# Performance work log

Measured on AMD Instinct MI355X. Metric: run time of the kernel, lower is better.

## Reference

```python
import jax, jax.numpy as jnp
import numpy as np

B, S, IN, OUT = 4, 2048, 4096, 11008


def setup_inputs() -> dict:
    key = jax.random.key(0)
    k1, k2, k3, k4 = jax.random.split(key, 4)
    x = jax.random.normal(k1, (B, S, IN), dtype=jnp.float32)
    # int8 weight codes (stored as int32 for portability; values in [0,127))
    weight_int8 = jax.random.randint(k2, (OUT, IN), 0, 127, dtype=jnp.int32)
    scale = jax.random.uniform(k3, (OUT,), dtype=jnp.float32) * 0.01 + 1e-4
    bias = jax.random.normal(k4, (OUT,), dtype=jnp.float32)
    return {"x": x, "weight_int8": weight_int8, "scale": scale, "bias": bias}


def reference(x, weight_int8, scale, bias):
    # dequantize: int8 codes -> fp, per-output-row scale (scale.view(-1,1) in torch)
    w = weight_int8.astype(jnp.float32) * scale[:, None]  # [OUT, IN]
    # F.linear(x, w, bias) == x @ w.T + bias
    out = jnp.einsum('bsi,oi->bso', x, w) + bias  # [B, S, OUT]
    return out
```

## Files before the change

### kernel.cpp

```cpp
#include <hip/hip_runtime.h>
#include <hip/hip_bf16.h>
#include <stdint.h>


#define MT 8192
#define KT 4096
#define NT 11008
#define NKT 32
#define MTILES 32
#define NTILES 86
#define CHUNK_A 32768
#define CHUNK_B 16384

typedef __attribute__((ext_vector_type(8))) short short8;
typedef __attribute__((ext_vector_type(4))) float f32x4;
typedef __attribute__((ext_vector_type(4))) int i32x4;
typedef __attribute__((ext_vector_type(16))) int i32x16;
typedef __attribute__((ext_vector_type(16))) char char16;

static __device__ __forceinline__ short f2bf(float f) {
  union { float f; unsigned u; } c; c.f = f;
  unsigned u = c.u;
  return (short)((u + 0x7fffu + ((u >> 16) & 1u)) >> 16);
}

__global__ __launch_bounds__(256) void quant_x_kernel(const float* __restrict__ in,
                                                      char* __restrict__ Aws,
                                                      float* __restrict__ sx) {
  const int m = blockIdx.x;
  const int t = threadIdx.x;
  const float* row = in + (size_t)m * KT + t * 16;
  f32x4 v[4];
  float mx = 0.f;
#pragma unroll
  for (int i = 0; i < 4; i++) {
    v[i] = *(const f32x4*)(row + i * 4);
#pragma unroll
    for (int j = 0; j < 4; j++) mx = fmaxf(mx, fabsf(v[i][j]));
  }
#pragma unroll
  for (int off = 32; off; off >>= 1) mx = fmaxf(mx, __shfl_xor(mx, off));
  __shared__ float smx[4];
  if ((t & 63) == 0) smx[t >> 6] = mx;
  __syncthreads();
  mx = fmaxf(fmaxf(smx[0], smx[1]), fmaxf(smx[2], smx[3]));
  const float inv = 127.0f / mx;
  if (t == 0) sx[m] = mx * (1.0f / 127.0f);
  char16 q;
#pragma unroll
  for (int i = 0; i < 4; i++)
#pragma unroll
    for (int j = 0; j < 4; j++) q[i * 4 + j] = (char)(int)rintf(v[i][j] * inv);
  const int kt = t >> 3, s = (t >> 1) & 3, hi = t & 1;
  const int lane = (m & 31) | (hi << 5);
  const int r32 = (m >> 5) & 7;
  *(char16*)(Aws + ((size_t)(m >> 8) * NKT + kt) * CHUNK_A +
             (r32 * 4 + s) * 1024 + lane * 16) = q;
}

__global__ __launch_bounds__(256) void cvt_w8_kernel(const int* __restrict__ in,
                                                     char* __restrict__ Bws) {
  const int n = blockIdx.x;
  const int t = threadIdx.x;
  const int* s_ = in + (size_t)n * KT + t * 16;
  char16 q;
#pragma unroll
  for (int i = 0; i < 4; i++) {
    i32x4 a = *(const i32x4*)(s_ + i * 4);
#pragma unroll
    for (int j = 0; j < 4; j++) q[i * 4 + j] = (char)a[j];
  }
  const int kt = t >> 3, s = (t >> 1) & 3, hi = t & 1;
  const int lane = (n & 31) | (hi << 5);
  const int c32 = (n >> 5) & 3;
  *(char16*)(Bws + ((size_t)(n >> 7) * NKT + kt) * CHUNK_B +
             (c32 * 4 + s) * 1024 + lane * 16) = q;
}


#define GLD(chunk, j, ldsbase)                                                   \
  __builtin_amdgcn_global_load_lds(                                              \
      (const __attribute__((address_space(1))) void*)((chunk) + (j) * 4096 +     \
                                                      tid * 16),                 \
      (__attribute__((address_space(3))) void*)((ldsbase) + (j) * 4096 +         \
                                                wid * 1024),                     \
      16, 0, 0)

#define GLDA(chunk, dst)                                       \
  do {                                                         \
    GLD(chunk, 0, dst); GLD(chunk, 1, dst);                    \
    GLD(chunk, 2, dst); GLD(chunk, 3, dst);                    \
    GLD(chunk, 4, dst); GLD(chunk, 5, dst);                    \
    GLD(chunk, 6, dst); GLD(chunk, 7, dst);                    \
  } while (0)

#define BAR asm volatile("s_barrier" ::: "memory")
#define VMC0 asm volatile("s_waitcnt vmcnt(0)" ::: "memory")

#define LOADB(B_, src)                                         \
  do {                                                         \
    const char* bb_ = (src) + wc * 8192 + lane * 16;           \
    B_[0][0] = *(const i32x4*)(bb_);                           \
    B_[0][1] = *(const i32x4*)(bb_ + 1024);                    \
    B_[0][2] = *(const i32x4*)(bb_ + 2048);                    \
    B_[0][3] = *(const i32x4*)(bb_ + 3072);                    \
    B_[1][0] = *(const i32x4*)(bb_ + 4096);                    \
    B_[1][1] = *(const i32x4*)(bb_ + 5120);                    \
    B_[1][2] = *(const i32x4*)(bb_ + 6144);                    \
    B_[1][3] = *(const i32x4*)(bb_ + 7168);                    \
  } while (0)

#define LDSL(LAp, s, aset)                                     \
  do {                                                         \
    const char* a_ = (LAp) + albase + (s) * 1024;              \
    aset[0] = *(const i32x4*)(a_);                             \
    aset[1] = *(const i32x4*)(a_ + 4096);                      \
    aset[2] = *(const i32x4*)(a_ + 8192);                      \
    aset[3] = *(const i32x4*)(a_ + 12288);                     \
  } while (0)

#define MMS(aset, BC, s)                                                       \
  do {                                                                         \
    __builtin_amdgcn_s_setprio(1);                                             \
    _Pragma("unroll") for (int mb = 0; mb < 4; mb++)                           \
        _Pragma("unroll") for (int nb = 0; nb < 2; nb++)                       \
            acc[mb][nb] = __builtin_amdgcn_mfma_i32_32x32x32_i8(               \
                aset[mb], BC[nb][s], acc[mb][nb], 0, 0, 0);                    \
    __builtin_amdgcn_s_setprio(0);                                             \
  } while (0)

#define TILE_BODY(BC, BN_)                                                     \
  {                                                                            \
    const char* LA = Lsm + (t & 1) * 32768;                                    \
    if (t + 1 < NKT) LOADB(BN_, Bch + CHUNK_B);                                \
    LDSL(LA, 1, a1);                                                           \
    MMS(a0, BC, 0);                                                            \
    LDSL(LA, 2, a0);                                                           \
    MMS(a1, BC, 1);                                                            \
    LDSL(LA, 3, a1);                                                           \
    MMS(a0, BC, 2);                                                            \
    MMS(a1, BC, 3);                                                            \
    VMC0;                                                                      \
    BAR;                                                                       \
    if (t + 1 < NKT) {                                                         \
      const char* LAn = Lsm + ((t + 1) & 1) * 32768;                           \
      LDSL(LAn, 0, a0);                                                        \
      if (t + 2 < NKT) {                                                       \
        char* dA = Lsm + (t & 1) * 32768;                                      \
        GLDA(Ach + 2 * CHUNK_A, dA);                                           \
      }                                                                        \
    }                                                                          \
    Ach += CHUNK_A;                                                            \
    Bch += CHUNK_B;                                                            \
    ++t;                                                                       \
  }

__global__ __launch_bounds__(256, 2) void gemm_bless(
    const char* __restrict__ Aws, const char* __restrict__ Bws,
    const float* __restrict__ sx, const float* __restrict__ scale,
    const float* __restrict__ bias, float* __restrict__ out) {
  extern __shared__ char Lsm[];
  const int tid = threadIdx.x;
  const int lane = tid & 63;
  const int wid = tid >> 6;
  const int wr = wid >> 1;
  const int wc = wid & 1;

  const int bid = blockIdx.x;
  const int r = bid >> 3;
  const int mt = (bid & 7) * 4 + (r & 3);
  const int nt = r >> 2;

  const char* Ach = Aws + (size_t)mt * NKT * CHUNK_A;
  const char* Bch = Bws + (size_t)nt * NKT * CHUNK_B;

  const int albase = wr * 16384 + lane * 16;

  i32x16 acc[4][2] = {};
  i32x4 a0[4], a1[4], bA[2][4], bB[2][4];

  {
    GLDA(Ach, Lsm);
    LOADB(bA, Bch);
    VMC0;
    BAR;
    GLDA(Ach + CHUNK_A, Lsm + 32768);
    LDSL(Lsm, 0, a0);
  }

  for (int t = 0; t < NKT;) {
    TILE_BODY(bA, bB);
    TILE_BODY(bB, bA);
  }

  const int col_base = nt * 128 + wc * 64 + (lane & 31);
  const int row0 = mt * 256 + wr * 128 + ((lane >> 5) << 2);
#pragma unroll
  for (int mb = 0; mb < 4; mb++) {
    f32x4 sxq[4];
#pragma unroll
    for (int g = 0; g < 4; g++)
      sxq[g] = *(const f32x4*)(sx + row0 + mb * 32 + g * 8);
#pragma unroll
    for (int nb = 0; nb < 2; nb++) {
      const int n = col_base + nb * 32;
      const float sc = scale[n];
      const float bs = bias[n];
#pragma unroll
      for (int g = 0; g < 4; g++)
#pragma unroll
        for (int j = 0; j < 4; j++) {
          const int row = row0 + mb * 32 + g * 8 + j;
          out[(size_t)row * NT + n] =
              (float)acc[mb][nb][g * 4 + j] * (sxq[g][j] * sc) + bs;
        }
    }
  }
}

__global__ __launch_bounds__(256) void gemm_fallback(
    const float* __restrict__ Ap, const int* __restrict__ Bp,
    const float* __restrict__ scale, const float* __restrict__ bias,
    float* __restrict__ out) {
  __shared__ short ldsA[128 * 64];
  __shared__ short ldsB[128 * 64];
  const int tid = threadIdx.x;
  const int lane = tid & 63;
  const int wid = tid >> 6;
  const int nbn = NT / 128;
  const int cpx = ((MT / 128) * nbn) / 8;
  const int bid = blockIdx.x;
  const int wg = (bid & 7) * cpx + (bid >> 3);
  const int brow = (wg / nbn) * 128;
  const int bcol = (wg % nbn) * 128;
  const int wr = wid >> 1, wc = wid & 1;
  f32x4 acc[4][4] = {{{0.f, 0.f, 0.f, 0.f}}};
  const int srow = tid >> 3;
  const int sk8 = (tid & 7) * 8;
  for (int k0 = 0; k0 < KT; k0 += 64) {
    __syncthreads();
#pragma unroll
    for (int p = 0; p < 4; p++) {
      const int row = p * 32 + srow;
      const float* s = Ap + (size_t)(brow + row) * KT + k0 + sk8;
      f32x4 lo = *(const f32x4*)s;
      f32x4 hi = *(const f32x4*)(s + 4);
      short8 v;
#pragma unroll
      for (int j = 0; j < 4; j++) { v[j] = f2bf(lo[j]); v[4 + j] = f2bf(hi[j]); }
      int bo = (row * 64 + sk8) * 2;
      bo ^= ((row & 7) << 4);
      *(short8*)((char*)ldsA + bo) = v;
    }
#pragma unroll
    for (int p = 0; p < 4; p++) {
      const int row = p * 32 + srow;
      const int* s = Bp + (size_t)(bcol + row) * KT + k0 + sk8;
      i32x4 lo = *(const i32x4*)(s);
      i32x4 hi = *(const i32x4*)(s + 4);
      short8 v;
#pragma unroll
      for (int j = 0; j < 4; j++) { v[j] = f2bf((float)lo[j]); v[4 + j] = f2bf((float)hi[j]); }
      int bo = (row * 64 + sk8) * 2;
      bo ^= ((row & 7) << 4);
      *(short8*)((char*)ldsB + bo) = v;
    }
    __syncthreads();
#pragma unroll
    for (int kk = 0; kk < 2; kk++) {
      short8 af[4], bf2[4];
#pragma unroll
      for (int mi = 0; mi < 4; mi++) {
        const int row = wr * 64 + mi * 16 + (lane & 15);
        int bo = (row * 64 + kk * 32 + (lane >> 4) * 8) * 2;
        bo ^= ((row & 7) << 4);
        af[mi] = *(const short8*)((const char*)ldsA + bo);
      }
#pragma unroll
      for (int ni = 0; ni < 4; ni++) {
        const int row = wc * 64 + ni * 16 + (lane & 15);
        int bo = (row * 64 + kk * 32 + (lane >> 4) * 8) * 2;
        bo ^= ((row & 7) << 4);
        bf2[ni] = *(const short8*)((const char*)ldsB + bo);
      }
#pragma unroll
      for (int mi = 0; mi < 4; mi++)
#pragma unroll
        for (int ni = 0; ni < 4; ni++)
          acc[mi][ni] = __builtin_amdgcn_mfma_f32_16x16x32_bf16(af[mi], bf2[ni],
                                                                acc[mi][ni], 0, 0, 0);
    }
  }
#pragma unroll
  for (int ni = 0; ni < 4; ni++) {
    const int n = bcol + wc * 64 + ni * 16 + (lane & 15);
    const float sc = scale[n];
    const float bs = bias[n];
#pragma unroll
    for (int mi = 0; mi < 4; mi++) {
      const int m0 = brow + wr * 64 + mi * 16 + ((lane >> 4) << 2);
#pragma unroll
      for (int j = 0; j < 4; j++)
        out[(size_t)(m0 + j) * NT + n] = acc[mi][ni][j] * sc + bs;
    }
  }
}

extern "C" void kernel_launch(void* const* d_in, const int* in_sizes, int n_in,
                              void* d_out, int out_size, void* d_ws, size_t ws_size,
                              hipStream_t stream) {
  const float* x = (const float*)d_in[0];
  const int* w = (const int*)d_in[1];
  const float* scale = (const float*)d_in[2];
  const float* bias = (const float*)d_in[3];
  float* out = (float*)d_out;

  const size_t a_bytes = (size_t)MTILES * NKT * CHUNK_A;
  const size_t b_bytes = (size_t)NTILES * NKT * CHUNK_B;
  const size_t s_bytes = (size_t)MT * sizeof(float);

  if (ws_size >= a_bytes + b_bytes + s_bytes) {
    char* aw = (char*)d_ws;
    char* bw = aw + a_bytes;
    float* sx = (float*)(bw + b_bytes);
    quant_x_kernel<<<dim3(MT), dim3(256), 0, stream>>>(x, aw, sx);
    cvt_w8_kernel<<<dim3(NT), dim3(256), 0, stream>>>(w, bw);
    hipFuncSetAttribute((const void*)gemm_bless,
                        hipFuncAttributeMaxDynamicSharedMemorySize, 65536);
    gemm_bless<<<dim3(MTILES * NTILES), dim3(256), 65536, stream>>>(
        aw, bw, sx, scale, bias, out);
  } else {
    gemm_fallback<<<dim3((MT / 128) * (NT / 128)), dim3(256), 0, stream>>>(
        x, w, scale, bias, out);
  }
}
```

Before: 521.5 us.

## Replace LDS-staged A tiles with direct global-to-register loads for both operands

Removes the shared-memory staging of A (global_load_lds plus barriers). Each wave now loads its A and B fragments straight from global memory into registers, using a two-slot register double buffer interleaved with the MFMA groups. The aim is to drop the LDS round trip, barrier stalls and the 64KB shared memory allocation. In exchange, A is fetched once per wave rather than once per block, which doubles global/L1 traffic for A. Load latency is also hidden by only about two MFMA groups, and the final iterations prefetch past the end of each tile.

```diff
diff --git a/kernel.cpp b/kernel.cpp
--- a/kernel.cpp
+++ b/kernel.cpp
@@ -78,88 +78,32 @@
 }
 
 
-#define GLD(chunk, j, ldsbase)                                                   \
-  __builtin_amdgcn_global_load_lds(                                              \
-      (const __attribute__((address_space(1))) void*)((chunk) + (j) * 4096 +     \
-                                                      tid * 16),                 \
-      (__attribute__((address_space(3))) void*)((ldsbase) + (j) * 4096 +         \
-                                                wid * 1024),                     \
-      16, 0, 0)
-
-#define GLDA(chunk, dst)                                       \
-  do {                                                         \
-    GLD(chunk, 0, dst); GLD(chunk, 1, dst);                    \
-    GLD(chunk, 2, dst); GLD(chunk, 3, dst);                    \
-    GLD(chunk, 4, dst); GLD(chunk, 5, dst);                    \
-    GLD(chunk, 6, dst); GLD(chunk, 7, dst);                    \
+#define LOADSL(u, A_, B_)                                                \
+  do {                                                                   \
+    const char* ab_ = Abase + (((u) >> 2) * CHUNK_A + ((u)&3) * 1024);   \
+    A_[0] = *(const i32x4*)(ab_);                                        \
+    A_[1] = *(const i32x4*)(ab_ + 4096);                                 \
+    A_[2] = *(const i32x4*)(ab_ + 8192);                                 \
+    A_[3] = *(const i32x4*)(ab_ + 12288);                                \
+    const char* bb_ = Bbase + (((u) >> 2) * CHUNK_B + ((u)&3) * 1024);   \
+    B_[0] = *(const i32x4*)(bb_);                                        \
+    B_[1] = *(const i32x4*)(bb_ + 4096);                                 \
   } while (0)
 
-#define BAR asm volatile("s_barrier" ::: "memory")
-#define VMC0 asm volatile("s_waitcnt vmcnt(0)" ::: "memory")
-
-#define LOADB(B_, src)                                         \
-  do {                                                         \
-    const char* bb_ = (src) + wc * 8192 + lane * 16;           \
-    B_[0][0] = *(const i32x4*)(bb_);                           \
-    B_[0][1] = *(const i32x4*)(bb_ + 1024);                    \
-    B_[0][2] = *(const i32x4*)(bb_ + 2048);                    \
-    B_[0][3] = *(const i32x4*)(bb_ + 3072);                    \
-    B_[1][0] = *(const i32x4*)(bb_ + 4096);                    \
-    B_[1][1] = *(const i32x4*)(bb_ + 5120);                    \
-    B_[1][2] = *(const i32x4*)(bb_ + 6144);                    \
-    B_[1][3] = *(const i32x4*)(bb_ + 7168);                    \
-  } while (0)
-
-#define LDSL(LAp, s, aset)                                     \
-  do {                                                         \
-    const char* a_ = (LAp) + albase + (s) * 1024;              \
-    aset[0] = *(const i32x4*)(a_);                             \
-    aset[1] = *(const i32x4*)(a_ + 4096);                      \
-    aset[2] = *(const i32x4*)(a_ + 8192);                      \
-    aset[3] = *(const i32x4*)(a_ + 12288);                     \
-  } while (0)
-
-#define MMS(aset, BC, s)                                                       \
+#define MMS(A_, B_)                                                            \
   do {                                                                         \
     __builtin_amdgcn_s_setprio(1);                                             \
     _Pragma("unroll") for (int mb = 0; mb < 4; mb++)                           \
         _Pragma("unroll") for (int nb = 0; nb < 2; nb++)                       \
             acc[mb][nb] = __builtin_amdgcn_mfma_i32_32x32x32_i8(               \
-                aset[mb], BC[nb][s], acc[mb][nb], 0, 0, 0);                    \
+                A_[mb], B_[nb], acc[mb][nb], 0, 0, 0);                         \
     __builtin_amdgcn_s_setprio(0);                                             \
   } while (0)
 
-#define TILE_BODY(BC, BN_)                                                     \
-  {                                                                            \
-    const char* LA = Lsm + (t & 1) * 32768;                                    \
-    if (t + 1 < NKT) LOADB(BN_, Bch + CHUNK_B);                                \
-    LDSL(LA, 1, a1);                                                           \
-    MMS(a0, BC, 0);                                                            \
-    LDSL(LA, 2, a0);                                                           \
-    MMS(a1, BC, 1);                                                            \
-    LDSL(LA, 3, a1);                                                           \
-    MMS(a0, BC, 2);                                                            \
-    MMS(a1, BC, 3);                                                            \
-    VMC0;                                                                      \
-    BAR;                                                                       \
-    if (t + 1 < NKT) {                                                         \
-      const char* LAn = Lsm + ((t + 1) & 1) * 32768;                           \
-      LDSL(LAn, 0, a0);                                                        \
-      if (t + 2 < NKT) {                                                       \
-        char* dA = Lsm + (t & 1) * 32768;                                      \
-        GLDA(Ach + 2 * CHUNK_A, dA);                                           \
-      }                                                                        \
-    }                                                                          \
-    Ach += CHUNK_A;                                                            \
-    Bch += CHUNK_B;                                                            \
-    ++t;                                                                       \
-  }
-
-__global__ __launch_bounds__(256, 2) void gemm_bless(
+__global__ __launch_bounds__(256, 2) void gemm_nolds(
     const char* __restrict__ Aws, const char* __restrict__ Bws,
     const float* __restrict__ sx, const float* __restrict__ scale,
     const float* __restrict__ bias, float* __restrict__ out) {
-  extern __shared__ char Lsm[];
   const int tid = threadIdx.x;
   const int lane = tid & 63;
   const int wid = tid >> 6;
@@ -171,26 +115,21 @@
   const int mt = (bid & 7) * 4 + (r & 3);
   const int nt = r >> 2;
 
-  const char* Ach = Aws + (size_t)mt * NKT * CHUNK_A;
-  const char* Bch = Bws + (size_t)nt * NKT * CHUNK_B;
-
-  const int albase = wr * 16384 + lane * 16;
+  const char* Abase = Aws + (size_t)mt * NKT * CHUNK_A + wr * 16384 + lane * 16;
+  const char* Bbase = Bws + (size_t)nt * NKT * CHUNK_B + wc * 8192 + lane * 16;
 
   i32x16 acc[4][2] = {};
-  i32x4 a0[4], a1[4], bA[2][4], bB[2][4];
-
-  {
-    GLDA(Ach, Lsm);
-    LOADB(bA, Bch);
-    VMC0;
-    BAR;
-    GLDA(Ach + CHUNK_A, Lsm + 32768);
-    LDSL(Lsm, 0, a0);
-  }
-
-  for (int t = 0; t < NKT;) {
-    TILE_BODY(bA, bB);
-    TILE_BODY(bB, bA);
+  i32x4 aP[4], bP[2], aQ[4], bQ[2];
+
+  LOADSL(0, aP, bP);
+  LOADSL(1, aQ, bQ);
+
+  for (int t = 0; t < NKT; ++t) {
+    const int u = t * 4;
+    MMS(aP, bP);  LOADSL(u + 2, aP, bP);
+    MMS(aQ, bQ);  LOADSL(u + 3, aQ, bQ);
+    MMS(aP, bP);  LOADSL(u + 4, aP, bP);
+    MMS(aQ, bQ);  LOADSL(u + 5, aQ, bQ);
   }
 
   const int col_base = nt * 128 + wc * 64 + (lane & 31);
@@ -325,9 +264,7 @@
     float* sx = (float*)(bw + b_bytes);
     quant_x_kernel<<<dim3(MT), dim3(256), 0, stream>>>(x, aw, sx);
     cvt_w8_kernel<<<dim3(NT), dim3(256), 0, stream>>>(w, bw);
-    hipFuncSetAttribute((const void*)gemm_bless,
-                        hipFuncAttributeMaxDynamicSharedMemorySize, 65536);
-    gemm_bless<<<dim3(MTILES * NTILES), dim3(256), 65536, stream>>>(
+    gemm_nolds<<<dim3(MTILES * NTILES), dim3(256), 0, stream>>>(
         aw, bw, sx, scale, bias, out);
   } else {
     gemm_fallback<<<dim3((MT / 128) * (NT / 128)), dim3(256), 0, stream>>>(
```

Measured after the change: 540.2 us. 1.04x slower.

## Swap GEMM tile shape to 128x256 and stream B per k-slice

Applied to the files above, without the earlier changes.

The int8 GEMM tile changes from 256 rows by 128 columns to 128 rows by 256 columns. The workspace layouts of quantized x and weights are rearranged to match. Only the smaller A chunk is staged through double-buffered LDS, which halves LDS use. B fragments are now loaded from global memory per k-slice, interleaved with the MFMAs, and a partial vmcnt wait keeps loads in flight across the barrier. The aim is lower LDS pressure and better latency hiding, at the cost of more direct global B traffic per wave and an extra barrier per k-step.

```diff
diff --git a/kernel.cpp b/kernel.cpp
--- a/kernel.cpp
+++ b/kernel.cpp
@@ -7,10 +7,10 @@
 #define KT 4096
 #define NT 11008
 #define NKT 32
-#define MTILES 32
-#define NTILES 86
-#define CHUNK_A 32768
-#define CHUNK_B 16384
+#define ATILES 64
+#define BTILES 43
+#define CHUNK_A 16384
+#define CHUNK_B 32768
 
 typedef __attribute__((ext_vector_type(8))) short short8;
 typedef __attribute__((ext_vector_type(4))) float f32x4;
@@ -53,8 +53,8 @@
     for (int j = 0; j < 4; j++) q[i * 4 + j] = (char)(int)rintf(v[i][j] * inv);
   const int kt = t >> 3, s = (t >> 1) & 3, hi = t & 1;
   const int lane = (m & 31) | (hi << 5);
-  const int r32 = (m >> 5) & 7;
-  *(char16*)(Aws + ((size_t)(m >> 8) * NKT + kt) * CHUNK_A +
+  const int r32 = (m >> 5) & 3;
+  *(char16*)(Aws + ((size_t)(m >> 7) * NKT + kt) * CHUNK_A +
              (r32 * 4 + s) * 1024 + lane * 16) = q;
 }
 
@@ -72,8 +72,8 @@
   }
   const int kt = t >> 3, s = (t >> 1) & 3, hi = t & 1;
   const int lane = (n & 31) | (hi << 5);
-  const int c32 = (n >> 5) & 3;
-  *(char16*)(Bws + ((size_t)(n >> 7) * NKT + kt) * CHUNK_B +
+  const int c32 = (n >> 5) & 7;
+  *(char16*)(Bws + ((size_t)(n >> 8) * NKT + kt) * CHUNK_B +
              (c32 * 4 + s) * 1024 + lane * 16) = q;
 }
 
@@ -90,24 +90,19 @@
   do {                                                         \
     GLD(chunk, 0, dst); GLD(chunk, 1, dst);                    \
     GLD(chunk, 2, dst); GLD(chunk, 3, dst);                    \
-    GLD(chunk, 4, dst); GLD(chunk, 5, dst);                    \
-    GLD(chunk, 6, dst); GLD(chunk, 7, dst);                    \
   } while (0)
 
 #define BAR asm volatile("s_barrier" ::: "memory")
 #define VMC0 asm volatile("s_waitcnt vmcnt(0)" ::: "memory")
-
-#define LOADB(B_, src)                                         \
+#define VMC20 asm volatile("s_waitcnt vmcnt(20)" ::: "memory")
+
+#define LOADB_SL(B_, ct, s)                                    \
   do {                                                         \
-    const char* bb_ = (src) + wc * 8192 + lane * 16;           \
-    B_[0][0] = *(const i32x4*)(bb_);                           \
-    B_[0][1] = *(const i32x4*)(bb_ + 1024);                    \
-    B_[0][2] = *(const i32x4*)(bb_ + 2048);                    \
-    B_[0][3] = *(const i32x4*)(bb_ + 3072);                    \
-    B_[1][0] = *(const i32x4*)(bb_ + 4096);                    \
-    B_[1][1] = *(const i32x4*)(bb_ + 5120);                    \
-    B_[1][2] = *(const i32x4*)(bb_ + 6144);                    \
-    B_[1][3] = *(const i32x4*)(bb_ + 7168);                    \
+    const char* bb_ = Bbase + (size_t)(ct)*CHUNK_B + (s)*1024; \
+    B_[0] = *(const i32x4*)(bb_);                              \
+    B_[1] = *(const i32x4*)(bb_ + 4096);                       \
+    B_[2] = *(const i32x4*)(bb_ + 8192);                       \
+    B_[3] = *(const i32x4*)(bb_ + 12288);                      \
   } while (0)
 
 #define LDSL(LAp, s, aset)                                     \
@@ -115,47 +110,19 @@
     const char* a_ = (LAp) + albase + (s) * 1024;              \
     aset[0] = *(const i32x4*)(a_);                             \
     aset[1] = *(const i32x4*)(a_ + 4096);                      \
-    aset[2] = *(const i32x4*)(a_ + 8192);                      \
-    aset[3] = *(const i32x4*)(a_ + 12288);                     \
   } while (0)
 
-#define MMS(aset, BC, s)                                                       \
+#define MMS(aset, bsl)                                                         \
   do {                                                                         \
     __builtin_amdgcn_s_setprio(1);                                             \
-    _Pragma("unroll") for (int mb = 0; mb < 4; mb++)                           \
-        _Pragma("unroll") for (int nb = 0; nb < 2; nb++)                       \
+    _Pragma("unroll") for (int mb = 0; mb < 2; mb++)                           \
+        _Pragma("unroll") for (int nb = 0; nb < 4; nb++)                       \
             acc[mb][nb] = __builtin_amdgcn_mfma_i32_32x32x32_i8(               \
-                aset[mb], BC[nb][s], acc[mb][nb], 0, 0, 0);                    \
+                aset[mb], bsl[nb], acc[mb][nb], 0, 0, 0);                      \
     __builtin_amdgcn_s_setprio(0);                                             \
   } while (0)
 
-#define TILE_BODY(BC, BN_)                                                     \
-  {                                                                            \
-    const char* LA = Lsm + (t & 1) * 32768;                                    \
-    if (t + 1 < NKT) LOADB(BN_, Bch + CHUNK_B);                                \
-    LDSL(LA, 1, a1);                                                           \
-    MMS(a0, BC, 0);                                                            \
-    LDSL(LA, 2, a0);                                                           \
-    MMS(a1, BC, 1);                                                            \
-    LDSL(LA, 3, a1);                                                           \
-    MMS(a0, BC, 2);                                                            \
-    MMS(a1, BC, 3);                                                            \
-    VMC0;                                                                      \
-    BAR;                                                                       \
-    if (t + 1 < NKT) {                                                         \
-      const char* LAn = Lsm + ((t + 1) & 1) * 32768;                           \
-      LDSL(LAn, 0, a0);                                                        \
-      if (t + 2 < NKT) {                                                       \
-        char* dA = Lsm + (t & 1) * 32768;                                      \
-        GLDA(Ach + 2 * CHUNK_A, dA);                                           \
-      }                                                                        \
-    }                                                                          \
-    Ach += CHUNK_A;                                                            \
-    Bch += CHUNK_B;                                                            \
-    ++t;                                                                       \
-  }
-
-__global__ __launch_bounds__(256, 2) void gemm_bless(
+__global__ __launch_bounds__(256, 2) void gemm_r11(
     const char* __restrict__ Aws, const char* __restrict__ Bws,
     const float* __restrict__ sx, const float* __restrict__ scale,
     const float* __restrict__ bias, float* __restrict__ out) {
@@ -167,42 +134,67 @@
   const int wc = wid & 1;
 
   const int bid = blockIdx.x;
-  const int r = bid >> 3;
-  const int mt = (bid & 7) * 4 + (r & 3);
-  const int nt = r >> 2;
+  const int g8 = bid & 7;
+  const int r8 = bid >> 3;
+  const int mt = g8 * 8 + (r8 & 7);
+  const int nt = r8 >> 3;
 
   const char* Ach = Aws + (size_t)mt * NKT * CHUNK_A;
-  const char* Bch = Bws + (size_t)nt * NKT * CHUNK_B;
-
-  const int albase = wr * 16384 + lane * 16;
-
-  i32x16 acc[4][2] = {};
-  i32x4 a0[4], a1[4], bA[2][4], bB[2][4];
+  const char* Bbase = Bws + (size_t)nt * NKT * CHUNK_B + wc * 16384 + lane * 16;
+
+  const int albase = wr * 8192 + lane * 16;
+
+  i32x16 acc[2][4] = {};
+  i32x4 a0[2], a1[2];
+  i32x4 b0[4], b1[4], b2[4], b3[4];
 
   {
     GLDA(Ach, Lsm);
-    LOADB(bA, Bch);
+    LOADB_SL(b0, 0, 0);
+    LOADB_SL(b1, 0, 1);
+    LOADB_SL(b2, 0, 2);
+    LOADB_SL(b3, 0, 3);
     VMC0;
     BAR;
-    GLDA(Ach + CHUNK_A, Lsm + 32768);
+    GLDA(Ach + CHUNK_A, Lsm + 16384);
     LDSL(Lsm, 0, a0);
   }
 
-  for (int t = 0; t < NKT;) {
-    TILE_BODY(bA, bB);
-    TILE_BODY(bB, bA);
-  }
-
-  const int col_base = nt * 128 + wc * 64 + (lane & 31);
-  const int row0 = mt * 256 + wr * 128 + ((lane >> 5) << 2);
-#pragma unroll
-  for (int mb = 0; mb < 4; mb++) {
+  for (int t = 0; t < NKT; ++t) {
+    const char* LA = Lsm + (t & 1) * 16384;
+
+    LDSL(LA, 1, a1);
+    MMS(a0, b0);  LOADB_SL(b0, t + 1, 0);
+    LDSL(LA, 2, a0);
+    MMS(a1, b1);  LOADB_SL(b1, t + 1, 1);
+    LDSL(LA, 3, a1);
+    MMS(a0, b2);  LOADB_SL(b2, t + 1, 2);
+    MMS(a1, b3);  LOADB_SL(b3, t + 1, 3);
+
+    BAR;
+    if (t + 2 < NKT) {
+      char* dA = Lsm + (t & 1) * 16384;
+      GLDA(Ach + 2 * CHUNK_A, dA);
+    }
+    if (t < NKT - 2) { VMC20; } else { VMC0; }
+    BAR;
+    if (t + 1 < NKT) {
+      const char* LAn = Lsm + ((t + 1) & 1) * 16384;
+      LDSL(LAn, 0, a0);
+    }
+    Ach += CHUNK_A;
+  }
+
+  const int col_base = nt * 256 + wc * 128 + (lane & 31);
+  const int row0 = mt * 128 + wr * 64 + ((lane >> 5) << 2);
+#pragma unroll
+  for (int mb = 0; mb < 2; mb++) {
     f32x4 sxq[4];
 #pragma unroll
     for (int g = 0; g < 4; g++)
       sxq[g] = *(const f32x4*)(sx + row0 + mb * 32 + g * 8);
 #pragma unroll
-    for (int nb = 0; nb < 2; nb++) {
+    for (int nb = 0; nb < 4; nb++) {
       const int n = col_base + nb * 32;
       const float sc = scale[n];
       const float bs = bias[n];
@@ -315,8 +307,8 @@
   const float* bias = (const float*)d_in[3];
   float* out = (float*)d_out;
 
-  const size_t a_bytes = (size_t)MTILES * NKT * CHUNK_A;
-  const size_t b_bytes = (size_t)NTILES * NKT * CHUNK_B;
+  const size_t a_bytes = (size_t)ATILES * NKT * CHUNK_A;
+  const size_t b_bytes = (size_t)BTILES * NKT * CHUNK_B;
   const size_t s_bytes = (size_t)MT * sizeof(float);
 
   if (ws_size >= a_bytes + b_bytes + s_bytes) {
@@ -325,9 +317,9 @@
     float* sx = (float*)(bw + b_bytes);
     quant_x_kernel<<<dim3(MT), dim3(256), 0, stream>>>(x, aw, sx);
     cvt_w8_kernel<<<dim3(NT), dim3(256), 0, stream>>>(w, bw);
-    hipFuncSetAttribute((const void*)gemm_bless,
-                        hipFuncAttributeMaxDynamicSharedMemorySize, 65536);
-    gemm_bless<<<dim3(MTILES * NTILES), dim3(256), 65536, stream>>>(
+    hipFuncSetAttribute((const void*)gemm_r11,
+                        hipFuncAttributeMaxDynamicSharedMemorySize, 32768);
+    gemm_r11<<<dim3(ATILES * BTILES), dim3(256), 32768, stream>>>(
         aw, bw, sx, scale, bias, out);
   } else {
     gemm_fallback<<<dim3((MT / 128) * (NT / 128)), dim3(256), 0, stream>>>(
```

Result: faster. 510.7 us (-2.1%).
